# Kernel tuning notes

Measured on AMD Instinct MI355X. Metric: run time of the kernel, lower is better.

## Reference

```python
import jax, jax.numpy as jnp
import numpy as np
import itertools

K, N, T, BS = 64, 128, 2, 128
LLR_MAX = 100.0


def _mod2(x):
    # values are small non-negative integers stored as floats
    return x - 2.0 * jnp.floor(x * 0.5)


def _dist(llr, c_hat):
    # llr: [bs, n], c_hat: [bs, P, n] -> [bs, P]
    # LLR-based distance: mean_n log(1 + exp(llr * (1 - 2c)))
    return jnp.mean(jax.nn.softplus(llr[:, None, :] * (1.0 - 2.0 * c_hat)), axis=2)


def _find_mrb(gm):
    # Gaussian elimination over GF(2) with data-dependent pivot columns.
    bs, k, n = gm.shape

    def body(idx_c, carry):
        gm, piv = carry
        row = jnp.take(gm, idx_c, axis=1)                                   # [bs, n]
        idx_p = jnp.argmax(row, axis=-1)                                    # [bs] pivot col
        r = jnp.take_along_axis(gm, idx_p[:, None, None], axis=2)[..., 0]   # [bs, k] pivot column
        r = jnp.where(jnp.arange(k)[None, :] == idx_c, 0.0, r)              # zero own row
        gm = _mod2(gm + r[:, :, None] * row[:, None, :])                    # eliminate
        piv = piv.at[:, idx_c].set(idx_p)
        return gm, piv

    gm, idx_pivot = jax.lax.fori_loop(0, k, body, (gm, jnp.zeros((bs, k), jnp.int32)))
    # build column permutation: pivots first, then remaining (parity) columns
    idx = jnp.tile(jnp.arange(n, dtype=jnp.int32)[None, :], (bs, 1))
    idx = idx.at[jnp.arange(bs)[:, None], idx_pivot].add(n)
    idx_parity = jnp.argsort(idx, axis=1)[:, : n - k].astype(jnp.int32)
    idx_sort = jnp.concatenate([idx_pivot, idx_parity], axis=1)             # [bs, n]
    gm = jnp.take_along_axis(gm, idx_sort[:, None, :], axis=2)
    return gm, idx_sort


def setup_inputs():
    key = jax.random.key(0)
    k1, k2 = jax.random.split(key)
    llr = 4.0 * jax.random.normal(k1, (BS, N), dtype=jnp.float32)
    gm = jax.random.randint(k2, (K, N), 0, 2).astype(jnp.float32)  # binary generator matrix
    return {"llr": llr, "gm": gm}


def reference(llr, gm):
    bs, n = llr.shape
    k = gm.shape[0]
    llr_ch = jnp.clip(llr, -LLR_MAX, LLR_MAX)
    # sort by reliability (descending |llr|)
    idx_sort = jnp.argsort(-jnp.abs(llr_ch), axis=1).astype(jnp.int32)      # [bs, n]
    gm_b = jnp.broadcast_to(gm[None], (bs, k, n))
    gm_sort = jnp.take_along_axis(gm_b, idx_sort[:, None, :], axis=2)
    gm_mrb, idx_mrb = _find_mrb(gm_sort)
    idx_sort = jnp.take_along_axis(idx_sort, idx_mrb, axis=1)
    llr_sort = jnp.take_along_axis(llr_ch, idx_sort, axis=1)
    idx_sort_inv = jnp.argsort(idx_sort, axis=1)
    # hard-decide k most reliable bits and re-encode
    u_hd = jnp.where(llr_sort[:, :k] < 0, 1.0, 0.0)                         # [bs, k]
    c = _mod2(jnp.einsum('bk,bkn->bn', u_hd, gm_mrb))                       # [bs, n]
    d_best = _dist(llr_sort, c[:, None, :])[:, 0]
    c_hat_best = c
    for t_i in range(1, T + 1):
        ep = jnp.asarray(list(itertools.combinations(range(k), t_i)), dtype=jnp.int32)  # [P, t_i]
        e = jnp.sum(gm_mrb[:, ep], axis=2) + c[:, None, :]                  # [bs, P, n]
        c_cand = _mod2(e)
        d = _dist(llr_sort, c_cand)                                         # [bs, P]
        idx = jnp.argmin(d, axis=1)
        c_hat = jnp.take_along_axis(c_cand, idx[:, None, None], axis=1)[:, 0]
        d_min = jnp.take_along_axis(d, idx[:, None], axis=1)[:, 0]
        better = d_min < d_best
        c_hat_best = jnp.where(better[:, None], c_hat, c_hat_best)
        d_best = jnp.where(better, d_min, d_best)
    # undo the MRB column permutation
    return jnp.take_along_axis(c_hat_best, idx_sort_inv, axis=1)
```

## Files before the change

### kernel.cpp

```cpp
#include <hip/hip_runtime.h>
#include <stdint.h>
#include <float.h>

typedef unsigned long long u64;
typedef unsigned int u32;

#define KK 64
#define NN 128
#define NCAND 2081

__device__ __forceinline__ u64 rdlane64(u64 v, int l) {
    u32 lo = (u32)__builtin_amdgcn_readlane((int)(u32)v, l);
    u32 hi = (u32)__builtin_amdgcn_readlane((int)(u32)(v >> 32), l);
    return ((u64)hi << 32) | lo;
}
__device__ __forceinline__ int ffs128(u64 x0, u64 x1) {
    return x0 ? (__ffsll((long long)x0) - 1) : (x1 ? (63 + __ffsll((long long)x1)) : 0);
}
__device__ __forceinline__ bool bit128(u64 x0, u64 x1, int p) {
    u64 sel = (p < 64) ? x0 : x1;
    return ((sel >> (p & 63)) & 1ull) != 0;
}
__device__ __forceinline__ void pair_of(int e, int& i, int& j) {
    float si = sqrtf(4032.25f - 2.0f * (float)e);
    i = (int)(63.5f - si);
    i = (i < 0) ? 0 : ((i > 62) ? 62 : i);
    int off = (i * (127 - i)) >> 1;
    if (e < off) { --i; off = (i * (127 - i)) >> 1; }
    else { int off2 = ((i + 1) * (126 - i)) >> 1; if (e >= off2) { ++i; off = off2; } }
    j = e - off + i + 1;
}

__global__ __launch_bounds__(256, 1) void osd_kernel(
    const float* __restrict__ llr_g,
    const float* __restrict__ gm_g,
    float* __restrict__ out_g)
{
    const int b    = blockIdx.x;
    const int tid  = threadIdx.x;
    const int lane = tid & 63;
    const int wave = tid >> 6;

    __shared__ u32   gOr[KK][5];
    __shared__ float llr_ch[NN];
    __shared__ int   prt[NN][5];
    __shared__ float lrs[NN];
    __shared__ int   idx_sort[NN];
    __shared__ u32   gS[KK][5];
    __shared__ int   mrb[NN];
    __shared__ int   ocArr[NN];
    __shared__ float w[NN];
    __shared__ u32   RlB[KK][4];
    __shared__ float lut[16][257];
    __shared__ u64   sh_hb[2];
    __shared__ u32   sh_bm[4];
    __shared__ u64   sh_cw[2];
    __shared__ u64   wred[4];

    float lv0 = llr_g[b * NN + lane];
    float lv1 = llr_g[b * NN + 64 + lane];
    lv0 = fminf(fmaxf(lv0, -100.0f), 100.0f);
    lv1 = fminf(fmaxf(lv1, -100.0f), 100.0f);
    float a0 = fabsf(lv0), a1 = fabsf(lv1);

    float gv[32];
    #pragma unroll
    for (int hh = 0; hh < 32; ++hh)
        gv[hh] = gm_g[(32 * wave + hh) * 64 + lane];

    int r0p = 0, r1p = 0;
    {
        const int jb = 16 * wave;
        #pragma unroll
        for (int jj = 0; jj < 16; ++jj) {
            int j = jb + jj;
            float aj0 = __int_as_float(__builtin_amdgcn_readlane(__float_as_int(a0), j));
            float aj1 = __int_as_float(__builtin_amdgcn_readlane(__float_as_int(a1), j));
            r0p += (aj0 > a0) || (aj0 == a0 && j < lane);
            r0p += (aj1 > a0);
            r1p += (aj0 > a1) || (aj0 == a1);
            r1p += (aj1 > a1) || (aj1 == a1 && j < lane);
        }
    }
    prt[lane][wave]      = r0p;
    prt[64 + lane][wave] = r1p;
    if (wave == 0) {
        llr_ch[lane]      = lv0;
        llr_ch[64 + lane] = lv1;
    }
    #pragma unroll
    for (int hh = 0; hh < 32; ++hh) {
        int h = 32 * wave + hh;
        u64 m = __ballot(gv[hh] != 0.0f);
        if (lane == 0) {
            gOr[h >> 1][(h & 1) * 2]     = (u32)m;
            gOr[h >> 1][(h & 1) * 2 + 1] = (u32)(m >> 32);
        }
    }
    __syncthreads();

    if (tid < NN) {
        int r = prt[tid][0] + prt[tid][1] + prt[tid][2] + prt[tid][3];
        idx_sort[r] = tid;
        lrs[r] = llr_ch[tid];
    }
    __syncthreads();

    {
        u64 o0 = (u64)gOr[lane][0] | ((u64)gOr[lane][1] << 32);
        u64 o1 = (u64)gOr[lane][2] | ((u64)gOr[lane][3] << 32);
        u32 word = 0;
        const int jbase = 32 * wave;
        #pragma unroll 8
        for (int jj = 0; jj < 32; ++jj) {
            int c = idx_sort[jbase + jj];
            u32 bit = (u32)(((c < 64) ? (o0 >> c) : (o1 >> (c - 64))) & 1ull);
            word |= bit << jj;
        }
        gS[lane][wave] = word;
    }
    __syncthreads();

    if (wave == 0) {
        u64 g0 = (u64)gS[lane][0] | ((u64)gS[lane][1] << 32);
        u64 g1 = (u64)gS[lane][2] | ((u64)gS[lane][3] << 32);
        int pv = 0;
        #pragma unroll 4
        for (int t = 0; t < 16; ++t) {
            const int c0 = 4 * t, c1 = c0 + 1, c2 = c0 + 2, c3 = c0 + 3;
            u64 A0 = rdlane64(g0, c0), A1 = rdlane64(g1, c0);
            u64 B0 = rdlane64(g0, c1), B1 = rdlane64(g1, c1);
            u64 C0 = rdlane64(g0, c2), C1 = rdlane64(g1, c2);
            u64 D0 = rdlane64(g0, c3), D1 = rdlane64(g1, c3);
            int pA = ffs128(A0, A1);
            if (bit128(B0, B1, pA)) { B0 ^= A0; B1 ^= A1; }
            if (bit128(C0, C1, pA)) { C0 ^= A0; C1 ^= A1; }
            if (bit128(D0, D1, pA)) { D0 ^= A0; D1 ^= A1; }
            int pB = ffs128(B0, B1);
            if (bit128(C0, C1, pB)) { C0 ^= B0; C1 ^= B1; }
            if (bit128(D0, D1, pB)) { D0 ^= B0; D1 ^= B1; }
            int pC = ffs128(C0, C1);
            if (bit128(D0, D1, pC)) { D0 ^= C0; D1 ^= C1; }
            int pD = ffs128(D0, D1);
            bool mA = bit128(g0, g1, pA) && (lane != c0);
            g0 ^= mA ? A0 : 0ull;  g1 ^= mA ? A1 : 0ull;
            bool mB = bit128(g0, g1, pB) && (lane != c1);
            g0 ^= mB ? B0 : 0ull;  g1 ^= mB ? B1 : 0ull;
            bool mC = bit128(g0, g1, pC) && (lane != c2);
            g0 ^= mC ? C0 : 0ull;  g1 ^= mC ? C1 : 0ull;
            bool mD = bit128(g0, g1, pD) && (lane != c3);
            g0 ^= mD ? D0 : 0ull;  g1 ^= mD ? D1 : 0ull;
            pv = (lane == c0) ? pA : (lane == c1) ? pB
               : (lane == c2) ? pC : (lane == c3) ? pD : pv;
        }
        gS[lane][0] = (u32)g0;
        gS[lane][1] = (u32)(g0 >> 32);
        gS[lane][2] = (u32)g1;
        gS[lane][3] = (u32)(g1 >> 32);

        u64 m0 = (pv < 64) ? (1ull << pv) : 0ull;
        u64 m1 = (pv >= 64) ? (1ull << (pv - 64)) : 0ull;
        #pragma unroll
        for (int off = 32; off; off >>= 1) {
            m0 |= __shfl_xor(m0, off);
            m1 |= __shfl_xor(m1, off);
        }
        u64 N0 = ~m0, N1 = ~m1;
        u64 below = (1ull << lane) - 1;
        int q0 = __popcll(N0 & below);
        int q1 = __popcll(N0) + __popcll(N1 & below);
        mrb[lane] = pv;
        if (((N0 >> lane) & 1ull) && q0 < 64) mrb[64 + q0] = lane;
        if (((N1 >> lane) & 1ull) && q1 < 64) mrb[64 + q1] = 64 + lane;
    }
    __syncthreads();

    if (tid < NN) {
        int sc = mrb[tid];
        float f = lrs[sc];
        w[tid] = fabsf(f);
        ocArr[tid] = idx_sort[sc];
        u64 hbm = __ballot(f < 0.0f);
        if (lane == 0) sh_hb[wave] = hbm;
    }
    {
        u64 e0 = (u64)gS[lane][0] | ((u64)gS[lane][1] << 32);
        u64 e1 = (u64)gS[lane][2] | ((u64)gS[lane][3] << 32);
        u32 word = 0;
        const int jbase = 32 * wave;
        #pragma unroll 8
        for (int jj = 0; jj < 32; ++jj) {
            int c = mrb[jbase + jj];
            u32 bit = (u32)(((c < 64) ? (e0 >> c) : (e1 >> (c - 64))) & 1ull);
            word |= bit << jj;
        }
        RlB[lane][wave] = word;
    }
    __syncthreads();

    if (wave == 0) {
        u64 hb0 = sh_hb[0];
        u64 R0 = (u64)RlB[lane][0] | ((u64)RlB[lane][1] << 32);
        u64 R1 = (u64)RlB[lane][2] | ((u64)RlB[lane][3] << 32);
        u64 hbit = (hb0 >> lane) & 1ull;
        u64 v0 = hbit ? R0 : 0ull;
        u64 v1 = hbit ? R1 : 0ull;
        #pragma unroll
        for (int off = 32; off; off >>= 1) {
            v0 ^= __shfl_xor(v0, off);
            v1 ^= __shfl_xor(v1, off);
        }
        if (lane == 0) {
            sh_cw[0] = v0; sh_cw[1] = v1;
            u64 bmA = v0 ^ hb0, bmB = v1 ^ sh_hb[1];
            sh_bm[0] = (u32)bmA; sh_bm[1] = (u32)(bmA >> 32);
            sh_bm[2] = (u32)bmB; sh_bm[3] = (u32)(bmB >> 32);
        }
    }
    {
        int p = tid >> 4;
        int t = tid & 15;
        const float* wp = &w[p * 8];
        float wv0 = wp[0], wv1 = wp[1], wv2 = wp[2], wv3 = wp[3];
        float wv4 = wp[4], wv5 = wp[5], wv6 = wp[6], wv7 = wp[7];
        float st = ((t & 1) ? wv4 : 0.0f) + ((t & 2) ? wv5 : 0.0f)
                 + ((t & 4) ? wv6 : 0.0f) + ((t & 8) ? wv7 : 0.0f);
        float* lrow = &lut[p][t << 4];
        #pragma unroll
        for (int lo = 0; lo < 16; ++lo)
            lrow[lo] = st + ((lo & 1) ? wv0 : 0.0f) + ((lo & 2) ? wv1 : 0.0f)
                          + ((lo & 4) ? wv2 : 0.0f) + ((lo & 8) ? wv3 : 0.0f);
    }
    __syncthreads();

#define SUM16(x0,x1,x2,x3) \
    (((lut[0][(x0) & 255]          + lut[1][((x0) >> 8) & 255])   \
    + (lut[2][((x0) >> 16) & 255]  + lut[3][(x0) >> 24]))         \
    + ((lut[4][(x1) & 255]         + lut[5][((x1) >> 8) & 255])   \
    + (lut[6][((x1) >> 16) & 255]  + lut[7][(x1) >> 24]))         \
    + ((lut[8][(x2) & 255]         + lut[9][((x2) >> 8) & 255])   \
    + (lut[10][((x2) >> 16) & 255] + lut[11][(x2) >> 24]))        \
    + ((lut[12][(x3) & 255]        + lut[13][((x3) >> 8) & 255])  \
    + (lut[14][((x3) >> 16) & 255] + lut[15][(x3) >> 24])))

    u32 bm0 = sh_bm[0], bm1 = sh_bm[1], bm2 = sh_bm[2], bm3 = sh_bm[3];
    float bestS = -1.0f;
    int bestId  = 0x7fffffff;
    if (tid <= 64) {
        u32 x0 = bm0, x1 = bm1, x2 = bm2, x3 = bm3;
        if (tid >= 1) {
            const u32* rp = &RlB[tid - 1][0];
            x0 ^= rp[0]; x1 ^= rp[1]; x2 ^= rp[2]; x3 ^= rp[3];
        }
        bestS = SUM16(x0, x1, x2, x3);
        bestId = tid;
    }
    {
        int e    = (tid * 2016) >> 8;
        int eEnd = ((tid + 1) * 2016) >> 8;
        int i, j;
        pair_of(e, i, j);
        const u32* rp = &RlB[i][0];
        u32 bi0 = bm0 ^ rp[0], bi1 = bm1 ^ rp[1], bi2 = bm2 ^ rp[2], bi3 = bm3 ^ rp[3];
        while (e < eEnd) {
            const u32* rj = &RlB[j][0];
            u32 x0 = bi0 ^ rj[0], x1 = bi1 ^ rj[1], x2 = bi2 ^ rj[2], x3 = bi3 ^ rj[3];
            float s = SUM16(x0, x1, x2, x3);
            int id = 65 + e;
            if (s > bestS || (s == bestS && id < bestId)) { bestS = s; bestId = id; }
            ++e; ++j;
            if (j == 64) {
                ++i; j = i + 1;
                const u32* rn = &RlB[i][0];
                bi0 = bm0 ^ rn[0]; bi1 = bm1 ^ rn[1]; bi2 = bm2 ^ rn[2]; bi3 = bm3 ^ rn[3];
            }
        }
    }
    u64 key = ((u64)(u32)__float_as_int(bestS) << 32)
            | (u32)(0x7fffffff - bestId);
    #pragma unroll
    for (int off = 32; off; off >>= 1) {
        u64 ok = __shfl_xor(key, off);
        key = (ok > key) ? ok : key;
    }
    if (lane == 0) wred[wave] = key;
    __syncthreads();

    if (tid < NN) {
        u64 ka = wred[0], kb = wred[1], kc = wred[2], kd = wred[3];
        u64 km = ka > kb ? ka : kb;
        u64 kn = kc > kd ? kc : kd;
        u64 kk = km > kn ? km : kn;
        int bId = 0x7fffffff - (int)(u32)(kk & 0xffffffffull);
        u64 c0 = sh_cw[0], c1 = sh_cw[1];
        if (bId >= 65) {
            int i, j;
            pair_of(bId - 65, i, j);
            c0 ^= ((u64)RlB[i][0] | ((u64)RlB[i][1] << 32))
                ^ ((u64)RlB[j][0] | ((u64)RlB[j][1] << 32));
            c1 ^= ((u64)RlB[i][2] | ((u64)RlB[i][3] << 32))
                ^ ((u64)RlB[j][2] | ((u64)RlB[j][3] << 32));
        } else if (bId >= 1) {
            int i = bId - 1;
            c0 ^= (u64)RlB[i][0] | ((u64)RlB[i][1] << 32);
            c1 ^= (u64)RlB[i][2] | ((u64)RlB[i][3] << 32);
        }
        u64 bit = (tid < 64) ? ((c0 >> tid) & 1ull) : ((c1 >> (tid - 64)) & 1ull);
        out_g[b * NN + ocArr[tid]] = (float)bit;
    }
#undef SUM16
}

extern "C" void kernel_launch(void* const* d_in, const int* in_sizes, int n_in,
                              void* d_out, int out_size, void* d_ws, size_t ws_size,
                              hipStream_t stream) {
    const float* llr = (const float*)d_in[0];
    const float* gm  = (const float*)d_in[1];
    float* out       = (float*)d_out;
    int bs = in_sizes[0] / NN;
    osd_kernel<<<bs, 256, 0, stream>>>(llr, gm, out);
}
```

Before: 23.70 us.

## Drop MRB column permutation and build LUT concurrently with codeword reduction

The kernel no longer builds the explicit MRB column permutation (mrb, ocArr, w) or repacks the reduced rows into permuted order. Hard decisions, LUT weights and candidate codewords now stay in the reliability-sorted column domain, and the output is scattered through idx_sort directly. This relies on the distance being invariant to column order. It removes two block barriers and a bit-gather loop. Wave 0 computes the base codeword while the other three waves build the lookup table in parallel, trading even work distribution across waves for fewer serialized phases.

```diff
diff --git a/kernel.cpp b/kernel.cpp
--- a/kernel.cpp
+++ b/kernel.cpp
@@ -47,12 +47,8 @@
     __shared__ float lrs[NN];
     __shared__ int   idx_sort[NN];
     __shared__ u32   gS[KK][5];
-    __shared__ int   mrb[NN];
-    __shared__ int   ocArr[NN];
-    __shared__ float w[NN];
-    __shared__ u32   RlB[KK][4];
+    __shared__ __align__(16) u32 RlB[KK][4];
     __shared__ float lut[16][257];
-    __shared__ u64   sh_hb[2];
     __shared__ u32   sh_bm[4];
     __shared__ u64   sh_cw[2];
     __shared__ u64   wred[4];
@@ -153,58 +149,17 @@
             pv = (lane == c0) ? pA : (lane == c1) ? pB
                : (lane == c2) ? pC : (lane == c3) ? pD : pv;
         }
-        gS[lane][0] = (u32)g0;
-        gS[lane][1] = (u32)(g0 >> 32);
-        gS[lane][2] = (u32)g1;
-        gS[lane][3] = (u32)(g1 >> 32);
-
-        u64 m0 = (pv < 64) ? (1ull << pv) : 0ull;
-        u64 m1 = (pv >= 64) ? (1ull << (pv - 64)) : 0ull;
-        #pragma unroll
-        for (int off = 32; off; off >>= 1) {
-            m0 |= __shfl_xor(m0, off);
-            m1 |= __shfl_xor(m1, off);
-        }
-        u64 N0 = ~m0, N1 = ~m1;
-        u64 below = (1ull << lane) - 1;
-        int q0 = __popcll(N0 & below);
-        int q1 = __popcll(N0) + __popcll(N1 & below);
-        mrb[lane] = pv;
-        if (((N0 >> lane) & 1ull) && q0 < 64) mrb[64 + q0] = lane;
-        if (((N1 >> lane) & 1ull) && q1 < 64) mrb[64 + q1] = 64 + lane;
-    }
-    __syncthreads();
-
-    if (tid < NN) {
-        int sc = mrb[tid];
-        float f = lrs[sc];
-        w[tid] = fabsf(f);
-        ocArr[tid] = idx_sort[sc];
-        u64 hbm = __ballot(f < 0.0f);
-        if (lane == 0) sh_hb[wave] = hbm;
-    }
-    {
-        u64 e0 = (u64)gS[lane][0] | ((u64)gS[lane][1] << 32);
-        u64 e1 = (u64)gS[lane][2] | ((u64)gS[lane][3] << 32);
-        u32 word = 0;
-        const int jbase = 32 * wave;
-        #pragma unroll 8
-        for (int jj = 0; jj < 32; ++jj) {
-            int c = mrb[jbase + jj];
-            u32 bit = (u32)(((c < 64) ? (e0 >> c) : (e1 >> (c - 64))) & 1ull);
-            word |= bit << jj;
-        }
-        RlB[lane][wave] = word;
-    }
-    __syncthreads();
-
-    if (wave == 0) {
-        u64 hb0 = sh_hb[0];
-        u64 R0 = (u64)RlB[lane][0] | ((u64)RlB[lane][1] << 32);
-        u64 R1 = (u64)RlB[lane][2] | ((u64)RlB[lane][3] << 32);
-        u64 hbit = (hb0 >> lane) & 1ull;
-        u64 v0 = hbit ? R0 : 0ull;
-        u64 v1 = hbit ? R1 : 0ull;
+        RlB[lane][0] = (u32)g0;
+        RlB[lane][1] = (u32)(g0 >> 32);
+        RlB[lane][2] = (u32)g1;
+        RlB[lane][3] = (u32)(g1 >> 32);
+
+        float s0 = lrs[lane], s1 = lrs[64 + lane];
+        u64 hd0 = __ballot(s0 < 0.0f);
+        u64 hd1 = __ballot(s1 < 0.0f);
+        u64 hbit = bit128(hd0, hd1, pv) ? 1ull : 0ull;
+        u64 v0 = hbit ? g0 : 0ull;
+        u64 v1 = hbit ? g1 : 0ull;
         #pragma unroll
         for (int off = 32; off; off >>= 1) {
             v0 ^= __shfl_xor(v0, off);
@@ -212,24 +167,29 @@
         }
         if (lane == 0) {
             sh_cw[0] = v0; sh_cw[1] = v1;
-            u64 bmA = v0 ^ hb0, bmB = v1 ^ sh_hb[1];
+            u64 bmA = v0 ^ hd0, bmB = v1 ^ hd1;
             sh_bm[0] = (u32)bmA; sh_bm[1] = (u32)(bmA >> 32);
             sh_bm[2] = (u32)bmB; sh_bm[3] = (u32)(bmB >> 32);
         }
-    }
-    {
-        int p = tid >> 4;
-        int t = tid & 15;
-        const float* wp = &w[p * 8];
-        float wv0 = wp[0], wv1 = wp[1], wv2 = wp[2], wv3 = wp[3];
-        float wv4 = wp[4], wv5 = wp[5], wv6 = wp[6], wv7 = wp[7];
-        float st = ((t & 1) ? wv4 : 0.0f) + ((t & 2) ? wv5 : 0.0f)
-                 + ((t & 4) ? wv6 : 0.0f) + ((t & 8) ? wv7 : 0.0f);
-        float* lrow = &lut[p][t << 4];
-        #pragma unroll
-        for (int lo = 0; lo < 16; ++lo)
-            lrow[lo] = st + ((lo & 1) ? wv0 : 0.0f) + ((lo & 2) ? wv1 : 0.0f)
-                          + ((lo & 4) ? wv2 : 0.0f) + ((lo & 8) ? wv3 : 0.0f);
+    } else {
+        int u = tid - 64;
+        #pragma unroll 2
+        for (int cell = u; cell < 256; cell += 192) {
+            int p = cell >> 4;
+            int t = cell & 15;
+            const float* wp = &lrs[p * 8];
+            float wv0 = fabsf(wp[0]), wv1 = fabsf(wp[1]);
+            float wv2 = fabsf(wp[2]), wv3 = fabsf(wp[3]);
+            float wv4 = fabsf(wp[4]), wv5 = fabsf(wp[5]);
+            float wv6 = fabsf(wp[6]), wv7 = fabsf(wp[7]);
+            float st = ((t & 1) ? wv4 : 0.0f) + ((t & 2) ? wv5 : 0.0f)
+                     + ((t & 4) ? wv6 : 0.0f) + ((t & 8) ? wv7 : 0.0f);
+            float* lrow = &lut[p][t << 4];
+            #pragma unroll
+            for (int lo = 0; lo < 16; ++lo)
+                lrow[lo] = st + ((lo & 1) ? wv0 : 0.0f) + ((lo & 2) ? wv1 : 0.0f)
+                              + ((lo & 4) ? wv2 : 0.0f) + ((lo & 8) ? wv3 : 0.0f);
+        }
     }
     __syncthreads();
 
@@ -306,7 +266,7 @@
             c1 ^= (u64)RlB[i][2] | ((u64)RlB[i][3] << 32);
         }
         u64 bit = (tid < 64) ? ((c0 >> tid) & 1ull) : ((c1 >> (tid - 64)) & 1ull);
-        out_g[b * NN + ocArr[tid]] = (float)bit;
+        out_g[b * NN + idx_sort[tid]] = (float)bit;
     }
 #undef SUM16
 }
```

Result: faster. 21.83 us (-7.9%).
